# Performance work log

Measured on AMD Instinct MI355X. Metric: run time of the kernel, lower is better.

## Reference

```python
import jax, jax.numpy as jnp
import numpy as np

ALPHA = 2.0
EPS = 1e-12  # F.normalize default eps


def setup_inputs() -> dict:
    key = jax.random.key(0)
    k1, k2 = jax.random.split(key)
    x = jax.random.normal(k1, (16, 512, 48, 48), dtype=jnp.float32)
    # 1x1 conv weight [out=1, in=C, 1, 1] flattened to [C], xavier-like scale
    w_query = jax.random.normal(k2, (512,), dtype=jnp.float32) * (2.0 / (512 + 1)) ** 0.5
    return {"x": x, "w_query": w_query}


def reference(x, w_query):
    b, c, h, w = x.shape
    n = h * w
    # attention map from detached x: 1x1 conv (dot over channels) + softplus -> [b, n]
    xd = jax.lax.stop_gradient(x)
    att = jax.nn.softplus(jnp.einsum('bchw,c->bhw', xd, w_query)).reshape(b, n)
    # L2-normalize over channel dim, flatten spatial -> [b, c, n]
    norm = jnp.sqrt(jnp.sum(x * x, axis=1, keepdims=True))
    flat = (x / jnp.maximum(norm, EPS)).reshape(b, c, n)
    # full NxN similarity, relu^alpha
    sim = jnp.einsum('bcn,bcm->bnm', flat, flat)  # [b, n, n]
    score = jnp.maximum(sim, 0.0) ** ALPHA
    # combine with attention map -> refine score per spatial location
    refine = jnp.einsum('bnm,bm->bn', score, att).reshape(b, 1, h, w)
    # weighted global average pool -> [b, c, 1, 1]
    return jnp.mean(x * refine, axis=(2, 3), keepdims=True)
```

## Files before the change

kernel.cpp:

```cpp
#include <hip/hip_runtime.h>

#define C_DIM 512
#define N_PIX 2304
#define B_DIM 16
#define K8    (C_DIM / 8)
#define K8_STRIDE (N_PIX * 8)
#define FB_STRIDE ((size_t)K8 * K8_STRIDE)
#define NB (B_DIM * N_PIX)
#define NSLICE 8

typedef float floatx4 __attribute__((ext_vector_type(4)));
typedef __bf16 bf16x8 __attribute__((ext_vector_type(8)));

static __device__ __forceinline__ unsigned short f2bf(float f) {
    unsigned u = __float_as_uint(f);
    return (unsigned short)((u + 0x7fffu + ((u >> 16) & 1u)) >> 16);
}

static __device__ __forceinline__ float softplus_stable(float z) {
    return (z > 0.f) ? (z + log1pf(expf(-z))) : log1pf(expf(z));
}

static __device__ __forceinline__ void load_lds16(const void* gp, void* l) {
    __builtin_amdgcn_global_load_lds(
        (const __attribute__((address_space(1))) unsigned int*)gp,
        (__attribute__((address_space(3))) unsigned int*)l, 16, 0, 0);
}

__global__ __launch_bounds__(256) void xcvt_kernel(const float* __restrict__ x,
                                                   const float* __restrict__ w,
                                                   unsigned short* __restrict__ F,
                                                   float* __restrict__ accd,
                                                   float* __restrict__ accs) {
    const int pg = blockIdx.x;
    const int cg = blockIdx.y;
    const int b  = pg / 18;
    const int p0 = (pg - b * 18) * 128;
    const int tid = threadIdx.x;
    const int p4  = tid & 31;
    const int k8g = tid >> 5;
    const int k8  = cg * 8 + k8g;
    const int p   = p0 + p4 * 4;

    const float* xb = x + (size_t)b * C_DIM * N_PIX;
    float4 d4 = {0.f, 0.f, 0.f, 0.f};
    float4 s4 = {0.f, 0.f, 0.f, 0.f};
    union { unsigned short u[4][8]; int4 v[4]; } cell;

    #pragma unroll
    for (int kk = 0; kk < 8; ++kk) {
        float4 xv = *(const float4*)(xb + (size_t)(k8 * 8 + kk) * N_PIX + p);
        const float wc = w[k8 * 8 + kk];
        d4.x = fmaf(xv.x, wc, d4.x);  s4.x = fmaf(xv.x, xv.x, s4.x);
        d4.y = fmaf(xv.y, wc, d4.y);  s4.y = fmaf(xv.y, xv.y, s4.y);
        d4.z = fmaf(xv.z, wc, d4.z);  s4.z = fmaf(xv.z, xv.z, s4.z);
        d4.w = fmaf(xv.w, wc, d4.w);  s4.w = fmaf(xv.w, xv.w, s4.w);
        cell.u[0][kk] = f2bf(xv.x);
        cell.u[1][kk] = f2bf(xv.y);
        cell.u[2][kk] = f2bf(xv.z);
        cell.u[3][kk] = f2bf(xv.w);
    }
    unsigned short* dst = F + (size_t)b * FB_STRIDE + (size_t)k8 * K8_STRIDE + (size_t)p * 8;
    #pragma unroll
    for (int i = 0; i < 4; ++i)
        *(int4*)(dst + i * 8) = cell.v[i];

    __shared__ float4 sd[NSLICE][32];
    __shared__ float4 ss[NSLICE][32];
    sd[k8g][p4] = d4;
    ss[k8g][p4] = s4;
    __syncthreads();

    if (tid < 32) {
        float4 d = sd[0][tid], s = ss[0][tid];
        #pragma unroll
        for (int j = 1; j < NSLICE; ++j) {
            float4 dj = sd[j][tid], sj = ss[j][tid];
            d.x += dj.x; d.y += dj.y; d.z += dj.z; d.w += dj.w;
            s.x += sj.x; s.y += sj.y; s.z += sj.z; s.w += sj.w;
        }
        const int o = b * N_PIX + p0 + tid * 4;
        *(float4*)(accd + (size_t)cg * NB + o) = d;
        *(float4*)(accs + (size_t)cg * NB + o) = s;
    }
}

__global__ __launch_bounds__(256) void finalize_kernel(const float* __restrict__ accd,
                                                       const float* __restrict__ accs,
                                                       float* __restrict__ g,
                                                       float* __restrict__ rn2,
                                                       float* __restrict__ refine) {
    const int bp = blockIdx.x * 256 + threadIdx.x;
    float d = 0.f, s = 0.f;
    #pragma unroll
    for (int i = 0; i < NSLICE; ++i) {
        d += accd[(size_t)i * NB + bp];
        s += accs[(size_t)i * NB + bp];
    }
    const float r2 = 1.0f / fmaxf(s, 1e-24f);
    g[bp]      = softplus_stable(d) * r2;
    rn2[bp]    = r2;
    refine[bp] = 0.f;
}

__global__ __launch_bounds__(256) void refine_kernel(const unsigned short* __restrict__ F,
                                                     const float* __restrict__ g,
                                                     float* __restrict__ refine) {
    const int id   = blockIdx.x;
    const int xcd  = id & 7;
    const int slot = id >> 3;
    const int hi   = (slot >= 171) ? 1 : 0;
    const int b    = xcd + 8 * hi;
    int t = slot - 171 * hi, bi = 0;
    while (t >= 18 - bi) { t -= 18 - bi; ++bi; }
    const int bj = bi + t;
    const int n0 = bi * 128;
    const int m0 = bj * 128;
    const bool mirror = (bi != bj);

    const unsigned short* Fb = F + (size_t)b * FB_STRIDE;
    const float* gb = g + b * N_PIX;

    __shared__ __align__(16) unsigned short As[4 * 128 * 8];
    __shared__ __align__(16) unsigned short Bs[4 * 128 * 8];

    const int tid  = threadIdx.x;
    const int lane = tid & 63;
    const int wave = tid >> 6;
    const int wr = wave >> 1, wc = wave & 1;
    const int quad = lane >> 4, lcol = lane & 15;

    floatx4 acc[4][4];
    #pragma unroll
    for (int i = 0; i < 4; ++i)
        #pragma unroll
        for (int j = 0; j < 4; ++j)
            acc[i][j] = (floatx4)0.f;

    const unsigned short* gA = Fb + (size_t)wave * K8_STRIDE + (size_t)n0 * 8 + lane * 8;
    const unsigned short* gB = Fb + (size_t)wave * K8_STRIDE + (size_t)m0 * 8 + lane * 8;

    for (int ck = 0; ck < 16; ++ck) {
        const unsigned short* sA = gA + (size_t)ck * (4 * K8_STRIDE);
        const unsigned short* sB = gB + (size_t)ck * (4 * K8_STRIDE);
        __syncthreads();
        load_lds16(sA,       &As[wave * 1024]);
        load_lds16(sA + 512, &As[wave * 1024 + 512]);
        load_lds16(sB,       &Bs[wave * 1024]);
        load_lds16(sB + 512, &Bs[wave * 1024 + 512]);
        __syncthreads();

        bf16x8 af[4], bfr[4];
        #pragma unroll
        for (int mi = 0; mi < 4; ++mi)
            af[mi] = *(const bf16x8*)&As[(quad * 128 + wr * 64 + mi * 16 + lcol) * 8];
        #pragma unroll
        for (int ni = 0; ni < 4; ++ni)
            bfr[ni] = *(const bf16x8*)&Bs[(quad * 128 + wc * 64 + ni * 16 + lcol) * 8];
        #pragma unroll
        for (int mi = 0; mi < 4; ++mi)
            #pragma unroll
            for (int ni = 0; ni < 4; ++ni)
                acc[mi][ni] = __builtin_amdgcn_mfma_f32_16x16x32_bf16(af[mi], bfr[ni], acc[mi][ni], 0, 0, 0);
    }

    float gC[4];
    #pragma unroll
    for (int ni = 0; ni < 4; ++ni)
        gC[ni] = gb[m0 + wc * 64 + ni * 16 + lcol];

    #pragma unroll
    for (int mi = 0; mi < 4; ++mi) {
        float part[4] = {0.f, 0.f, 0.f, 0.f};
        #pragma unroll
        for (int ni = 0; ni < 4; ++ni) {
            #pragma unroll
            for (int r = 0; r < 4; ++r) {
                float s = fmaxf(acc[mi][ni][r], 0.f);
                part[r] = fmaf(s * s, gC[ni], part[r]);
            }
        }
        #pragma unroll
        for (int r = 0; r < 4; ++r) {
            float v = part[r];
            v += __shfl_xor(v, 1);
            v += __shfl_xor(v, 2);
            v += __shfl_xor(v, 4);
            v += __shfl_xor(v, 8);
            if (lcol == 0)
                atomicAdd(&refine[b * N_PIX + n0 + wr * 64 + mi * 16 + quad * 4 + r], v);
        }
    }

    if (mirror) {
        float gR[4][4];
        #pragma unroll
        for (int mi = 0; mi < 4; ++mi)
            #pragma unroll
            for (int r = 0; r < 4; ++r)
                gR[mi][r] = gb[n0 + wr * 64 + mi * 16 + quad * 4 + r];

        #pragma unroll
        for (int ni = 0; ni < 4; ++ni) {
            float msum = 0.f;
            #pragma unroll
            for (int mi = 0; mi < 4; ++mi) {
                #pragma unroll
                for (int r = 0; r < 4; ++r) {
                    float s = fmaxf(acc[mi][ni][r], 0.f);
                    msum = fmaf(s * s, gR[mi][r], msum);
                }
            }
            msum += __shfl_xor(msum, 16);
            msum += __shfl_xor(msum, 32);
            if (quad == 0)
                atomicAdd(&refine[b * N_PIX + m0 + wc * 64 + ni * 16 + lcol], msum);
        }
    }
}

__global__ __launch_bounds__(256) void pool_kernel(const unsigned short* __restrict__ F,
                                                   const float* __restrict__ refine,
                                                   const float* __restrict__ rn2,
                                                   float* __restrict__ out) {
    const int lane = threadIdx.x & 63;
    const int wave = threadIdx.x >> 6;
    const int b  = blockIdx.x >> 6;
    const int k8 = blockIdx.x & 63;
    const unsigned short* Fr = F + (size_t)b * FB_STRIDE + (size_t)k8 * K8_STRIDE;
    const float* rf = refine + b * N_PIX;
    const float* r2 = rn2 + b * N_PIX;
    float s[8] = {0.f, 0.f, 0.f, 0.f, 0.f, 0.f, 0.f, 0.f};
    #pragma unroll
    for (int j = 0; j < 9; ++j) {
        const int n = (j * 4 + wave) * 64 + lane;
        bf16x8 fv = *(const bf16x8*)(Fr + (size_t)n * 8);
        float rr = rf[n] * r2[n];
        #pragma unroll
        for (int kk = 0; kk < 8; ++kk)
            s[kk] = fmaf((float)fv[kk], rr, s[kk]);
    }
    __shared__ float sred[4][8];
    #pragma unroll
    for (int kk = 0; kk < 8; ++kk) {
        float v = s[kk];
        #pragma unroll
        for (int off = 32; off > 0; off >>= 1) v += __shfl_down(v, off);
        if (lane == 0) sred[wave][kk] = v;
    }
    __syncthreads();
    if (threadIdx.x < 8) {
        const int kk = threadIdx.x;
        out[b * C_DIM + k8 * 8 + kk] =
            (sred[0][kk] + sred[1][kk] + sred[2][kk] + sred[3][kk]) * (1.0f / N_PIX);
    }
}

__global__ __launch_bounds__(256) void prep_kernel(const float* __restrict__ x,
                                                   const float* __restrict__ w,
                                                   float* __restrict__ rnorm,
                                                   float* __restrict__ att) {
    const int tid = threadIdx.x;
    const int px = tid & 63;
    const int cc = tid >> 6;
    const int pglob = blockIdx.x * 64 + px;
    const int b = pglob / N_PIX;
    const int p = pglob - b * N_PIX;

    const float* xb = x + (size_t)b * C_DIM * N_PIX + p;
    float dot = 0.f, sq = 0.f;
    #pragma unroll 4
    for (int c = cc * 128; c < cc * 128 + 128; ++c) {
        float v = xb[(size_t)c * N_PIX];
        dot = fmaf(v, w[c], dot);
        sq  = fmaf(v, v, sq);
    }
    __shared__ float sdot[4][64];
    __shared__ float ssq[4][64];
    sdot[cc][px] = dot;
    ssq[cc][px]  = sq;
    __syncthreads();
    if (cc == 0) {
        dot = sdot[0][px] + sdot[1][px] + sdot[2][px] + sdot[3][px];
        sq  = ssq[0][px]  + ssq[1][px]  + ssq[2][px]  + ssq[3][px];
        att[pglob] = softplus_stable(dot);
        rnorm[pglob] = 1.0f / fmaxf(sqrtf(sq), 1e-12f);
    }
}

__global__ __launch_bounds__(256) void refine_fallback(const float* __restrict__ x,
                                                       const float* __restrict__ rnorm,
                                                       const float* __restrict__ att,
                                                       float* __restrict__ refine) {
    const int b  = blockIdx.z;
    const int n0 = blockIdx.x * 128;
    const int m0 = blockIdx.y * 128;
    const float* xb = x + (size_t)b * C_DIM * N_PIX;
    const float* rn = rnorm + b * N_PIX;
    const float* ab = att + b * N_PIX;

    __shared__ __align__(16) unsigned short As[4 * 128 * 8];
    __shared__ __align__(16) unsigned short Bs[4 * 128 * 8];

    const int tid  = threadIdx.x;
    const int nl   = tid & 127;
    const int half = tid >> 7;
    const int lane = tid & 63;
    const int wave = tid >> 6;
    const int wr = wave >> 1, wc = wave & 1;
    const int quad = lane >> 4, lcol = lane & 15;

    const float rA = rn[n0 + nl];
    const float rB = rn[m0 + nl];

    floatx4 acc[4][4];
    #pragma unroll
    for (int i = 0; i < 4; ++i)
        #pragma unroll
        for (int j = 0; j < 4; ++j)
            acc[i][j] = (floatx4)0.f;

    for (int k0 = 0; k0 < C_DIM; k0 += 32) {
        const float* xa = xb + (size_t)(k0 + half * 16) * N_PIX;
        union { unsigned short u[16]; int4 v[2]; } ta, tb;
        #pragma unroll
        for (int j = 0; j < 16; ++j) {
            float va = xa[(size_t)j * N_PIX + n0 + nl];
            float vb = xa[(size_t)j * N_PIX + m0 + nl];
            ta.u[j] = f2bf(va * rA);
            tb.u[j] = f2bf(vb * rB);
        }
        __syncthreads();
        *(int4*)&As[((half * 2 + 0) * 128 + nl) * 8] = ta.v[0];
        *(int4*)&As[((half * 2 + 1) * 128 + nl) * 8] = ta.v[1];
        *(int4*)&Bs[((half * 2 + 0) * 128 + nl) * 8] = tb.v[0];
        *(int4*)&Bs[((half * 2 + 1) * 128 + nl) * 8] = tb.v[1];
        __syncthreads();

        bf16x8 af[4], bfr[4];
        #pragma unroll
        for (int mi = 0; mi < 4; ++mi)
            af[mi] = *(const bf16x8*)&As[(quad * 128 + wr * 64 + mi * 16 + lcol) * 8];
        #pragma unroll
        for (int ni = 0; ni < 4; ++ni)
            bfr[ni] = *(const bf16x8*)&Bs[(quad * 128 + wc * 64 + ni * 16 + lcol) * 8];
        #pragma unroll
        for (int mi = 0; mi < 4; ++mi)
            #pragma unroll
            for (int ni = 0; ni < 4; ++ni)
                acc[mi][ni] = __builtin_amdgcn_mfma_f32_16x16x32_bf16(af[mi], bfr[ni], acc[mi][ni], 0, 0, 0);
    }

    float attv[4];
    #pragma unroll
    for (int ni = 0; ni < 4; ++ni)
        attv[ni] = ab[m0 + wc * 64 + ni * 16 + lcol];

    #pragma unroll
    for (int mi = 0; mi < 4; ++mi) {
        float part[4] = {0.f, 0.f, 0.f, 0.f};
        #pragma unroll
        for (int ni = 0; ni < 4; ++ni) {
            #pragma unroll
            for (int r = 0; r < 4; ++r) {
                float s = fmaxf(acc[mi][ni][r], 0.f);
                part[r] = fmaf(s * s, attv[ni], part[r]);
            }
        }
        #pragma unroll
        for (int r = 0; r < 4; ++r) {
            float v = part[r];
            v += __shfl_xor(v, 1);
            v += __shfl_xor(v, 2);
            v += __shfl_xor(v, 4);
            v += __shfl_xor(v, 8);
            if (lcol == 0)
                atomicAdd(&refine[b * N_PIX + n0 + wr * 64 + mi * 16 + quad * 4 + r], v);
        }
    }
}

__global__ __launch_bounds__(256) void pool_fallback(const float* __restrict__ x,
                                                     const float* __restrict__ refine,
                                                     float* __restrict__ out) {
    const int lane = threadIdx.x & 63;
    const int wave = threadIdx.x >> 6;
    const int gidx = blockIdx.x * 4 + wave;
    const int b = gidx >> 9;
    const float4* xr = (const float4*)(x + (size_t)gidx * N_PIX);
    const float4* rr = (const float4*)(refine + (size_t)b * N_PIX);
    float s = 0.f;
    #pragma unroll
    for (int j = 0; j < 9; ++j) {
        float4 xv = xr[j * 64 + lane];
        float4 rv = rr[j * 64 + lane];
        s += xv.x * rv.x + xv.y * rv.y + xv.z * rv.z + xv.w * rv.w;
    }
    #pragma unroll
    for (int off = 32; off > 0; off >>= 1) s += __shfl_down(s, off);
    if (lane == 0) out[gidx] = s * (1.0f / N_PIX);
}

extern "C" void kernel_launch(void* const* d_in, const int* in_sizes, int n_in,
                              void* d_out, int out_size, void* d_ws, size_t ws_size,
                              hipStream_t stream) {
    const float* x = (const float*)d_in[0];
    const float* w = (const float*)d_in[1];
    float* rn2    = (float*)d_ws;
    float* g      = rn2 + NB;
    float* refine = g + NB;
    float* accd   = refine + NB;
    float* accs   = accd + (size_t)NSLICE * NB;
    unsigned short* F = (unsigned short*)(accs + (size_t)NSLICE * NB);
    float* out    = (float*)d_out;

    const size_t need = (size_t)(3 + 2 * NSLICE) * NB * 4 + (size_t)B_DIM * FB_STRIDE * 2;

    if (ws_size >= need) {
        xcvt_kernel<<<dim3(288, NSLICE), 256, 0, stream>>>(x, w, F, accd, accs);
        finalize_kernel<<<dim3(NB / 256), 256, 0, stream>>>(accd, accs, g, rn2, refine);
        refine_kernel<<<dim3(171 * 16), 256, 0, stream>>>(F, g, refine);
        pool_kernel<<<dim3(B_DIM * K8), 256, 0, stream>>>(F, refine, rn2, out);
    } else {
        hipMemsetAsync(refine, 0, (size_t)NB * 4, stream);
        prep_kernel<<<dim3(NB / 64), 256, 0, stream>>>(x, w, rn2, g);
        refine_fallback<<<dim3(18, 18, B_DIM), 256, 0, stream>>>(x, rn2, g, refine);
        pool_fallback<<<dim3(B_DIM * C_DIM / 4), 256, 0, stream>>>(x, refine, out);
    }
}
```

Measured before the change: 188.8 us.

## Fold finalize kernel into refine and xcvt, apply row norm before atomics

Removes the separate finalize kernel. Each refine block now reduces the per-slice dot and norm partials for its 256 rows and columns itself, and keeps g and 1/norm² in shared memory. The 1/norm² factor is applied to partial sums before the atomicAdd, so the pool kernel no longer reads rn2. Zeroing of refine moves into xcvt, and refine gets launch bounds of 3 blocks per CU. This saves a launch and some global traffic, at the cost of redundant partial reductions across refine blocks (each row is reduced about 18 times).

```diff
diff --git a/kernel.cpp b/kernel.cpp
--- a/kernel.cpp
+++ b/kernel.cpp
@@ -31,7 +31,8 @@
                                                    const float* __restrict__ w,
                                                    unsigned short* __restrict__ F,
                                                    float* __restrict__ accd,
-                                                   float* __restrict__ accs) {
+                                                   float* __restrict__ accs,
+                                                   float* __restrict__ refine) {
     const int pg = blockIdx.x;
     const int cg = blockIdx.y;
     const int b  = pg / 18;
@@ -82,30 +83,15 @@
         const int o = b * N_PIX + p0 + tid * 4;
         *(float4*)(accd + (size_t)cg * NB + o) = d;
         *(float4*)(accs + (size_t)cg * NB + o) = s;
-    }
-}
-
-__global__ __launch_bounds__(256) void finalize_kernel(const float* __restrict__ accd,
-                                                       const float* __restrict__ accs,
-                                                       float* __restrict__ g,
-                                                       float* __restrict__ rn2,
-                                                       float* __restrict__ refine) {
-    const int bp = blockIdx.x * 256 + threadIdx.x;
-    float d = 0.f, s = 0.f;
-    #pragma unroll
-    for (int i = 0; i < NSLICE; ++i) {
-        d += accd[(size_t)i * NB + bp];
-        s += accs[(size_t)i * NB + bp];
-    }
-    const float r2 = 1.0f / fmaxf(s, 1e-24f);
-    g[bp]      = softplus_stable(d) * r2;
-    rn2[bp]    = r2;
-    refine[bp] = 0.f;
-}
-
-__global__ __launch_bounds__(256) void refine_kernel(const unsigned short* __restrict__ F,
-                                                     const float* __restrict__ g,
-                                                     float* __restrict__ refine) {
+        if (cg == 0)
+            *(float4*)(refine + o) = (float4){0.f, 0.f, 0.f, 0.f};
+    }
+}
+
+__global__ __launch_bounds__(256, 3) void refine_kernel(const unsigned short* __restrict__ F,
+                                                        const float* __restrict__ accd,
+                                                        const float* __restrict__ accs,
+                                                        float* __restrict__ refine) {
     const int id   = blockIdx.x;
     const int xcd  = id & 7;
     const int slot = id >> 3;
@@ -119,16 +105,31 @@
     const bool mirror = (bi != bj);
 
     const unsigned short* Fb = F + (size_t)b * FB_STRIDE;
-    const float* gb = g + b * N_PIX;
 
     __shared__ __align__(16) unsigned short As[4 * 128 * 8];
     __shared__ __align__(16) unsigned short Bs[4 * 128 * 8];
+    __shared__ float sg_g[256];
+    __shared__ float sg_r2[256];
 
     const int tid  = threadIdx.x;
     const int lane = tid & 63;
     const int wave = tid >> 6;
     const int wr = wave >> 1, wc = wave & 1;
     const int quad = lane >> 4, lcol = lane & 15;
+
+    {
+        const int p = (tid < 128) ? (n0 + tid) : (m0 + (tid - 128));
+        const int o = b * N_PIX + p;
+        float d = 0.f, s = 0.f;
+        #pragma unroll
+        for (int i = 0; i < NSLICE; ++i) {
+            d += accd[(size_t)i * NB + o];
+            s += accs[(size_t)i * NB + o];
+        }
+        const float r2 = 1.0f / fmaxf(s, 1e-24f);
+        sg_g[tid]  = softplus_stable(d) * r2;
+        sg_r2[tid] = r2;
+    }
 
     floatx4 acc[4][4];
     #pragma unroll
@@ -167,7 +168,7 @@
     float gC[4];
     #pragma unroll
     for (int ni = 0; ni < 4; ++ni)
-        gC[ni] = gb[m0 + wc * 64 + ni * 16 + lcol];
+        gC[ni] = sg_g[128 + wc * 64 + ni * 16 + lcol];
 
     #pragma unroll
     for (int mi = 0; mi < 4; ++mi) {
@@ -187,8 +188,10 @@
             v += __shfl_xor(v, 2);
             v += __shfl_xor(v, 4);
             v += __shfl_xor(v, 8);
-            if (lcol == 0)
-                atomicAdd(&refine[b * N_PIX + n0 + wr * 64 + mi * 16 + quad * 4 + r], v);
+            if (lcol == 0) {
+                const int row = wr * 64 + mi * 16 + quad * 4 + r;
+                atomicAdd(&refine[b * N_PIX + n0 + row], v * sg_r2[row]);
+            }
         }
     }
 
@@ -198,7 +201,7 @@
         for (int mi = 0; mi < 4; ++mi)
             #pragma unroll
             for (int r = 0; r < 4; ++r)
-                gR[mi][r] = gb[n0 + wr * 64 + mi * 16 + quad * 4 + r];
+                gR[mi][r] = sg_g[wr * 64 + mi * 16 + quad * 4 + r];
 
         #pragma unroll
         for (int ni = 0; ni < 4; ++ni) {
@@ -213,15 +216,16 @@
             }
             msum += __shfl_xor(msum, 16);
             msum += __shfl_xor(msum, 32);
-            if (quad == 0)
-                atomicAdd(&refine[b * N_PIX + m0 + wc * 64 + ni * 16 + lcol], msum);
+            if (quad == 0) {
+                const int col = wc * 64 + ni * 16 + lcol;
+                atomicAdd(&refine[b * N_PIX + m0 + col], msum * sg_r2[128 + col]);
+            }
         }
     }
 }
 
 __global__ __launch_bounds__(256) void pool_kernel(const unsigned short* __restrict__ F,
                                                    const float* __restrict__ refine,
-                                                   const float* __restrict__ rn2,
                                                    float* __restrict__ out) {
     const int lane = threadIdx.x & 63;
     const int wave = threadIdx.x >> 6;
@@ -229,13 +233,12 @@
     const int k8 = blockIdx.x & 63;
     const unsigned short* Fr = F + (size_t)b * FB_STRIDE + (size_t)k8 * K8_STRIDE;
     const float* rf = refine + b * N_PIX;
-    const float* r2 = rn2 + b * N_PIX;
     float s[8] = {0.f, 0.f, 0.f, 0.f, 0.f, 0.f, 0.f, 0.f};
     #pragma unroll
     for (int j = 0; j < 9; ++j) {
         const int n = (j * 4 + wave) * 64 + lane;
         bf16x8 fv = *(const bf16x8*)(Fr + (size_t)n * 8);
-        float rr = rf[n] * r2[n];
+        float rr = rf[n];
         #pragma unroll
         for (int kk = 0; kk < 8; ++kk)
             s[kk] = fmaf((float)fv[kk], rr, s[kk]);
@@ -406,25 +409,26 @@
                               hipStream_t stream) {
     const float* x = (const float*)d_in[0];
     const float* w = (const float*)d_in[1];
-    float* rn2    = (float*)d_ws;
-    float* g      = rn2 + NB;
-    float* refine = g + NB;
+    float* out    = (float*)d_out;
+
+    float* refine = (float*)d_ws;
     float* accd   = refine + NB;
     float* accs   = accd + (size_t)NSLICE * NB;
     unsigned short* F = (unsigned short*)(accs + (size_t)NSLICE * NB);
-    float* out    = (float*)d_out;
-
-    const size_t need = (size_t)(3 + 2 * NSLICE) * NB * 4 + (size_t)B_DIM * FB_STRIDE * 2;
+
+    const size_t need = (size_t)(1 + 2 * NSLICE) * NB * 4 + (size_t)B_DIM * FB_STRIDE * 2;
 
     if (ws_size >= need) {
-        xcvt_kernel<<<dim3(288, NSLICE), 256, 0, stream>>>(x, w, F, accd, accs);
-        finalize_kernel<<<dim3(NB / 256), 256, 0, stream>>>(accd, accs, g, rn2, refine);
-        refine_kernel<<<dim3(171 * 16), 256, 0, stream>>>(F, g, refine);
-        pool_kernel<<<dim3(B_DIM * K8), 256, 0, stream>>>(F, refine, rn2, out);
+        xcvt_kernel<<<dim3(288, NSLICE), 256, 0, stream>>>(x, w, F, accd, accs, refine);
+        refine_kernel<<<dim3(171 * 16), 256, 0, stream>>>(F, accd, accs, refine);
+        pool_kernel<<<dim3(B_DIM * K8), 256, 0, stream>>>(F, refine, out);
     } else {
-        hipMemsetAsync(refine, 0, (size_t)NB * 4, stream);
-        prep_kernel<<<dim3(NB / 64), 256, 0, stream>>>(x, w, rn2, g);
-        refine_fallback<<<dim3(18, 18, B_DIM), 256, 0, stream>>>(x, rn2, g, refine);
-        pool_fallback<<<dim3(B_DIM * C_DIM / 4), 256, 0, stream>>>(x, refine, out);
-    }
-}
+        float* rnorm = (float*)d_ws;
+        float* att   = rnorm + NB;
+        float* refF  = att + NB;
+        hipMemsetAsync(refF, 0, (size_t)NB * 4, stream);
+        prep_kernel<<<dim3(NB / 64), 256, 0, stream>>>(x, w, rnorm, att);
+        refine_fallback<<<dim3(18, 18, B_DIM), 256, 0, stream>>>(x, rnorm, att, refF);
+        pool_fallback<<<dim3(B_DIM * C_DIM / 4), 256, 0, stream>>>(x, refF, out);
+    }
+}
```

Result: no change. 186.5 us (-1.2%).
